# Performance work log

Hardware: AMD Instinct MI355X
Metric: run time of the kernel (lower is better)

Reference implementation:

```python
import jax, jax.numpy as jnp
import numpy as np

N_HASHES = 8
BUCKET_SIZE = 64


def setup_inputs() -> dict:
    key = jax.random.key(0)
    k1, k2, k3 = jax.random.split(key, 3)
    B, S, D = 16, 4096, 64
    n_buckets = S // BUCKET_SIZE  # 64
    qk = jax.random.normal(k1, (B, S, D), jnp.float32)
    v = jax.random.normal(k2, (B, S, D), jnp.float32)
    # random rotations (shared across batch, per hash round): (1, D, n_hashes, n_buckets//2)
    rotations = jax.random.normal(k3, (1, D, N_HASHES, n_buckets // 2), jnp.float32)
    return {"qk": qk, "v": v, "rotations": rotations}


def _look_one_back(x):
    # concat each chunk with the previous chunk (wrap-around), along the within-chunk axis
    x_extra = jnp.roll(x, 1, axis=1)
    return jnp.concatenate([x, x_extra], axis=2)


def _lsh_attention(qk, v, rotations):
    B, S, D = qk.shape
    n_buckets = S // BUCKET_SIZE

    # ---- hash_vectors ----
    rot = jnp.broadcast_to(rotations, (B, D, N_HASHES, n_buckets // 2))
    rotated = jnp.einsum('btf,bfhi->bhti', qk, rot)           # [B, H, S, nb/2]
    rotated = jnp.concatenate([rotated, -rotated], axis=-1)    # [B, H, S, nb]
    buckets = jnp.argmax(rotated, axis=-1)                     # [B, H, S]
    offsets = (jnp.arange(N_HASHES) * n_buckets).reshape(1, -1, 1)
    buckets = (buckets + offsets).reshape(B, -1)               # [B, H*S]

    # ---- sort by (bucket, position) ----
    total = N_HASHES * S
    ticker = jnp.arange(total)
    buckets_and_t = S * buckets + (ticker % S)[None, :]        # unique keys
    sticker = jnp.argsort(buckets_and_t, axis=-1)              # sort order
    undo_sort = jnp.argsort(sticker, axis=-1)

    st = sticker % S                                           # original positions
    sqk = jnp.take_along_axis(qk, st[..., None], axis=1)       # [B, H*S, D]
    sv = jnp.take_along_axis(v, st[..., None], axis=1)

    chunk_size = N_HASHES * n_buckets                          # number of chunks
    bq_t = st.reshape(B, chunk_size, -1)                       # [B, C, bs]
    bqk = sqk.reshape(B, chunk_size, -1, D)                    # [B, C, bs, D]
    bv = sv.reshape(B, chunk_size, -1, D)

    bq = bqk
    bk = bqk / jnp.clip(jnp.linalg.norm(bqk, axis=-1, keepdims=True), 1e-12)

    bk = _look_one_back(bk)                                    # [B, C, 2*bs, D]
    bv = _look_one_back(bv)
    bkv_t = _look_one_back(bq_t)                               # [B, C, 2*bs]

    dots = jnp.einsum('bhie,bhje->bhij', bq, bk) * (D ** -0.5)  # [B, C, bs, 2*bs]

    # mask self-attention (token attending to itself)
    self_mask = bq_t[:, :, :, None] == bkv_t[:, :, None, :]
    dots = jnp.where(self_mask, jnp.float32(-1e5), dots)

    lse = jax.nn.logsumexp(dots, axis=-1, keepdims=True)
    probs = jnp.exp(dots - lse)
    bo = jnp.einsum('buij,buje->buie', probs, bv)              # [B, C, bs, D]

    so = bo.reshape(B, -1, D)                                  # [B, H*S, D]
    slogits = lse.reshape(B, -1)                               # [B, H*S]

    # unsort back to original order
    o = jnp.take_along_axis(so, undo_sort[..., None], axis=1)
    logits = jnp.take_along_axis(slogits, undo_sort, axis=1)

    o = o.reshape(B, N_HASHES, S, D)
    logits = logits.reshape(B, N_HASHES, S, 1)

    # combine hash rounds by normalized logsumexp weights
    w = jnp.exp(logits - jax.nn.logsumexp(logits, axis=1, keepdims=True))
    out = jnp.sum(o * w, axis=1)                               # [B, S, D]
    return out, buckets


def reference(qk, v, rotations):
    return _lsh_attention(qk, v, rotations)
```

## Files before the change

kernel.cpp:

```cpp
#include <hip/hip_runtime.h>
#include <hip/hip_bf16.h>
#include <math.h>

#define B 16
#define S 4096
#define D 64
#define NH 8
#define NBUCK 64
#define CHUNKS 512
#define BS 64

#define GAP_MFMA 0.03f

typedef __attribute__((ext_vector_type(8))) short s8_t;
typedef __attribute__((ext_vector_type(8))) _Float16 h8_t;
typedef __attribute__((ext_vector_type(4))) float f4_t;
typedef __attribute__((ext_vector_type(2))) unsigned int u32x2;

__device__ inline unsigned short f16_rne(float x) {
    union { _Float16 f; unsigned short u; } cv;
    cv.f = (_Float16)x;
    return cv.u;
}
__device__ inline unsigned int pack_f16_pair(float x0, float x1) {
    return (unsigned int)f16_rne(x0) | ((unsigned int)f16_rne(x1) << 16);
}
__device__ inline unsigned int pack_trunc(float x0, float x1) {
    return __builtin_amdgcn_perm(__float_as_uint(x1), __float_as_uint(x0),
                                 0x07060302u);
}
__device__ inline unsigned short bf16_trunc(float x) {
    return (unsigned short)(__float_as_uint(x) >> 16);
}

#define BAR_LGKM() do {                                          \
    asm volatile("s_waitcnt lgkmcnt(0)" ::: "memory");           \
    __builtin_amdgcn_s_barrier();                                \
    asm volatile("" ::: "memory");                               \
} while (0)

template<int OFF>
__device__ inline u32x2 tr_read(unsigned int vaddr) {
    u32x2 d;
    asm volatile("ds_read_b64_tr_b16 %0, %1 offset:%c2"
                 : "=v"(d) : "v"(vaddr), "i"(OFF));
    return d;
}

#define HA_OFF 0
#define HQ_OFF 36864
#define HLDS_TOT 55296
#define HSTR 144

__global__ __launch_bounds__(256, 2) void hash_kernel(
    const float* __restrict__ qk, const float* __restrict__ rot,
    float* __restrict__ out_buckets, int* __restrict__ bucket_ws,
    unsigned char* __restrict__ flag_ws)
{
    __shared__ char lds[HLDS_TOT];
    int tid = threadIdx.x;
    int wg = blockIdx.x;
    int orig = ((wg & 7) << 6) + (wg >> 3);
    int b    = orig >> 5;
    int tile = orig & 31;
    int token0 = tile * 128;

    {
        char* arow = lds + HA_OFF + tid * HSTR;
        #pragma unroll 4
        for (int f = 0; f < 64; f += 2) {
            float r0 = rot[(size_t)f * 256 + tid];
            float r1 = rot[(size_t)(f + 1) * 256 + tid];
            *(unsigned int*)(arow + f * 2) = pack_f16_pair(r0, r1);
        }
    }
    {
        int wv0   = tid >> 6;
        int lane0 = tid & 63;
        int s_ = lane0 & 3;
        int rowA = wv0 * 32 + (lane0 >> 2);
        int rowB = rowA + 16;
        const float4* qA = (const float4*)(qk + ((size_t)b * S + token0 + rowA) * D);
        const float4* qB = (const float4*)(qk + ((size_t)b * S + token0 + rowB) * D);
        float4 a4[4], b4[4];
        #pragma unroll
        for (int n = 0; n < 4; ++n) { a4[n] = qA[n * 4 + s_]; b4[n] = qB[n * 4 + s_]; }

        char* qhA = lds + HQ_OFF + rowA * HSTR;
        char* qhB = lds + HQ_OFF + rowB * HSTR;
        #pragma unroll
        for (int n = 0; n < 4; ++n) {
            *(uint2*)(qhA + n * 32 + s_ * 8) =
                make_uint2(pack_f16_pair(a4[n].x, a4[n].y),
                           pack_f16_pair(a4[n].z, a4[n].w));
            *(uint2*)(qhB + n * 32 + s_ * 8) =
                make_uint2(pack_f16_pair(b4[n].x, b4[n].y),
                           pack_f16_pair(b4[n].z, b4[n].w));
        }
    }
    __syncthreads();

    int wv   = tid >> 6;
    int lane = tid & 63;
    int quad = lane >> 4;
    int cc   = lane & 15;

    for (int nt = 0; nt < 2; ++nt) {
        int ntg = wv * 2 + nt;
        const char* qr = lds + HQ_OFF + (ntg * 16 + cc) * HSTR + quad * 16;
        h8_t b0 = *(const h8_t*)(qr);
        h8_t b1 = *(const h8_t*)(qr + 64);

        float v1 = -3e38f, v2 = -3e38f;
        int i1 = 0;

        for (int mt = 0; mt < 16; ++mt) {
            const char* arow = lds + HA_OFF + (mt * 16 + cc) * HSTR + quad * 16;
            h8_t a0 = *(const h8_t*)(arow);
            h8_t a1 = *(const h8_t*)(arow + 64);
            f4_t acc = (f4_t){0.f, 0.f, 0.f, 0.f};
            acc = __builtin_amdgcn_mfma_f32_16x16x32_f16(a0, b0, acc, 0, 0, 0);
            acc = __builtin_amdgcn_mfma_f32_16x16x32_f16(a1, b1, acc, 0, 0, 0);

            if ((mt & 1) == 0) { v1 = -3e38f; v2 = -3e38f; i1 = 0; }
            int ibase = ((mt & 1) << 4) + (quad << 2);
            #pragma unroll
            for (int r = 0; r < 4; ++r) {
                float vp = acc[r];
                int ip = ibase + r;
                v2 = fmaxf(v2, fminf(vp, v1));
                if (vp > v1) { v1 = vp; i1 = ip; }
                float vn = -vp;
                v2 = fmaxf(v2, fminf(vn, v1));
                if (vn > v1) { v1 = vn; i1 = ip + 32; }
            }

            if (mt & 1) {
                #pragma unroll
                for (int off = 16; off <= 32; off <<= 1) {
                    float ov1 = __shfl_xor(v1, off, 64);
                    float ov2 = __shfl_xor(v2, off, 64);
                    int   oi1 = __shfl_xor(i1, off, 64);
                    float nv2 = fmaxf(fmaxf(v2, ov2), fminf(v1, ov1));
                    if (ov1 > v1) { v1 = ov1; i1 = oi1; }
                    v2 = nv2;
                }
                if (quad == 0) {
                    int h = mt >> 1;
                    int tok = token0 + ntg * 16 + cc;
                    size_t idx = (size_t)(b * NH + h) * S + tok;
                    bucket_ws[idx] = i1;
                    out_buckets[idx] = (float)(i1 + h * NBUCK);
                    flag_ws[idx] = (v1 - v2 < GAP_MFMA) ? 1 : 0;
                }
            }
        }
    }
}

__global__ __launch_bounds__(256) void hash_fixup_kernel(
    const float* __restrict__ qk, const float* __restrict__ rot,
    const unsigned char* __restrict__ flag_ws,
    float* __restrict__ out_buckets, int* __restrict__ bucket_ws)
{
    __shared__ int list[2048];
    __shared__ int cnt;
    int tid = threadIdx.x;
    if (tid == 0) cnt = 0;
    __syncthreads();

    int base = blockIdx.x * 2048;
    for (int i = tid; i < 2048; i += 256) {
        if (flag_ws[base + i]) {
            int slot = atomicAdd(&cnt, 1);
            list[slot] = base + i;
        }
    }
    __syncthreads();
    int n = cnt;

    for (int j = tid; j < n; j += 256) {
        int gid = list[j];
        int bh = gid >> 12, t = gid & (S - 1);
        int b = bh >> 3, h = bh & 7;
        const float* row = qk + ((size_t)b * S + t) * D;

        double acc[32];
        #pragma unroll
        for (int i = 0; i < 32; ++i) acc[i] = 0.0;
        for (int f = 0; f < 64; ++f) {
            double x = (double)row[f];
            const float* rr = rot + f * (NH * 32) + h * 32;
            #pragma unroll
            for (int i = 0; i < 32; ++i)
                acc[i] = __fma_rn(x, (double)rr[i], acc[i]);
        }
        double best = acc[0]; int bi = 0;
        double worst = acc[0]; int wi = 0;
        #pragma unroll
        for (int i = 1; i < 32; ++i) {
            if (acc[i] > best)  { best = acc[i]; bi = i; }
            if (acc[i] < worst) { worst = acc[i]; wi = i; }
        }
        int bucket = (-worst > best) ? (32 + wi) : bi;
        bucket_ws[gid] = bucket;
        out_buckets[gid] = (float)(bucket + h * NBUCK);
    }
}

__global__ __launch_bounds__(1024) void sort_kernel(
    const int* __restrict__ bucket_ws, int* __restrict__ st_ws)
{
    __shared__ int sb[S];
    __shared__ int hist[16][64];
    __shared__ int bpref[64];
    __shared__ int woff[16][64];

    int tid  = threadIdx.x;
    int wv   = tid >> 6;
    int lane = tid & 63;
    int base = blockIdx.x * S;

    hist[wv][lane] = 0;
    __syncthreads();

    int qbase = wv * 256;
    #pragma unroll
    for (int i = 0; i < 4; ++i) {
        int t = qbase + i * 64 + lane;
        int v = bucket_ws[base + t];
        sb[t] = v;
        atomicAdd(&hist[wv][v], 1);
    }
    __syncthreads();

    if (wv == 0) {
        int total = 0;
        #pragma unroll
        for (int w = 0; w < 16; ++w) total += hist[w][lane];
        int x = total;
        #pragma unroll
        for (int off = 1; off < 64; off <<= 1) {
            int y = __shfl_up(x, off, 64);
            if (lane >= off) x += y;
        }
        bpref[lane] = x - total;
    }
    __syncthreads();
    {
        int o = bpref[lane];
        #pragma unroll
        for (int w2 = 0; w2 < 16; ++w2) {
            if (w2 < wv) o += hist[w2][lane];
        }
        woff[wv][lane] = o;
    }
    __syncthreads();

    for (int g = 0; g < 4; ++g) {
        int t = qbase + g * 64 + lane;
        int v = sb[t];

        unsigned long long m = ~0ULL;
        #pragma unroll
        for (int bit = 0; bit < 6; ++bit) {
            unsigned long long bm = __ballot((v >> bit) & 1);
            m &= ((v >> bit) & 1) ? bm : ~bm;
        }
        unsigned long long below = (lane == 63) ? ~0ULL >> 1
                                 : ((1ULL << lane) - 1ULL);
        int rank = __popcll(m & below);
        int cnt  = __popcll(m);

        int pos = woff[wv][v] + rank;
        st_ws[base + pos] = t;

        if ((m & below) == 0ULL)
            woff[wv][v] += cnt;
    }
}

#define OFF_VT 18432
#define OFF_NRM 35840
#define OFF_TKX 36352
#define OFF_PINV 36864
#define LDS_TOT 37120
#define KSTRB 144
#define PSTRB 272

template<int KC>
__device__ inline void pv_step(const char* lds, unsigned vaddr,
                               int wv, int cc, int quad, f4_t* oaccT)
{
    s8_t pb = *(const s8_t*)(lds + (wv * 16 + cc) * PSTRB + KC * 64 + quad * 16);
    u32x2 t00 = tr_read<KC * 4352 +    0>(vaddr);
    u32x2 t01 = tr_read<KC * 4352 +  544>(vaddr);
    u32x2 t10 = tr_read<KC * 4352 + 1088>(vaddr);
    u32x2 t11 = tr_read<KC * 4352 + 1632>(vaddr);
    u32x2 t20 = tr_read<KC * 4352 + 2176>(vaddr);
    u32x2 t21 = tr_read<KC * 4352 + 2720>(vaddr);
    u32x2 t30 = tr_read<KC * 4352 + 3264>(vaddr);
    u32x2 t31 = tr_read<KC * 4352 + 3808>(vaddr);
    asm volatile("s_waitcnt lgkmcnt(0)" ::: "memory");
    __builtin_amdgcn_sched_barrier(0);
    union { u32x2 d[2]; s8_t s; } u0, u1, u2, u3;
    u0.d[0] = t00; u0.d[1] = t01;
    u1.d[0] = t10; u1.d[1] = t11;
    u2.d[0] = t20; u2.d[1] = t21;
    u3.d[0] = t30; u3.d[1] = t31;
    oaccT[0] = __builtin_amdgcn_mfma_f32_16x16x32_bf16(u0.s, pb, oaccT[0], 0, 0, 0);
    oaccT[1] = __builtin_amdgcn_mfma_f32_16x16x32_bf16(u1.s, pb, oaccT[1], 0, 0, 0);
    oaccT[2] = __builtin_amdgcn_mfma_f32_16x16x32_bf16(u2.s, pb, oaccT[2], 0, 0, 0);
    oaccT[3] = __builtin_amdgcn_mfma_f32_16x16x32_bf16(u3.s, pb, oaccT[3], 0, 0, 0);
}

__global__ __launch_bounds__(256, 4) void attn_kernel(
    const float* __restrict__ qk, const float* __restrict__ v,
    const int* __restrict__ st_ws,
    __hip_bfloat16* __restrict__ o_ws, float* __restrict__ logits_ws)
{
    __shared__ char lds[LDS_TOT];
    float* nrm_s  = (float*)(lds + OFF_NRM);
    int*   tkx    = (int*)(lds + OFF_TKX);
    float* pinv_s = (float*)(lds + OFF_PINV);

    int tid = threadIdx.x;
    int wg = blockIdx.x;
    int orig = ((wg & 7) << 10) + (wg >> 3);
    int c = orig & (CHUNKS - 1);
    int b = orig >> 9;
    int h = c >> 6;
    int sbase = b * (NH * S);
    int cprev = (c + CHUNKS - 1) & (CHUNKS - 1);

    int wv   = tid >> 6;
    int lane = tid & 63;
    int quad = lane >> 4;
    int cc   = lane & 15;
    int s_   = lane & 3;

    int rowA = wv * 32 + (lane >> 2);
    int rowB = rowA + 16;
    int chK  = (wv < 2) ? c : cprev;
    int tokKA = st_ws[sbase + chK * BS + (rowA & 63)];
    int tokKB = st_ws[sbase + chK * BS + (rowB & 63)];
    const float4* kpA = (const float4*)(qk + ((size_t)b * S + tokKA) * D);
    const float4* kpB = (const float4*)(qk + ((size_t)b * S + tokKB) * D);
    float4 kA4[4], kB4[4];
    #pragma unroll
    for (int n = 0; n < 4; ++n) { kA4[n] = kpA[n * 4 + s_]; kB4[n] = kpB[n * 4 + s_]; }

    int prA = wv * 32 + (lane >> 2);
    int prB = prA + 16;
    int ciA = ((prA & 3) << 4) | (prA >> 3);
    int ciB = ((prB & 3) << 4) | (prB >> 3);
    int chVA = (prA & 4) ? cprev : c;
    int chVB = (prB & 4) ? cprev : c;
    int tokVA = st_ws[sbase + chVA * BS + ciA];
    int tokVB = st_ws[sbase + chVB * BS + ciB];
    const float4* vpA = (const float4*)(v + ((size_t)b * S + tokVA) * D);
    const float4* vpB = (const float4*)(v + ((size_t)b * S + tokVB) * D);
    float4 vA4[4], vB4[4];
    #pragma unroll
    for (int n = 0; n < 4; ++n) { vA4[n] = vpA[n * 4 + s_]; vB4[n] = vpB[n * 4 + s_]; }

    {
        float ssA = 0.f, ssB = 0.f;
        #pragma unroll
        for (int n = 0; n < 4; ++n) {
            ssA += kA4[n].x*kA4[n].x + kA4[n].y*kA4[n].y
                 + kA4[n].z*kA4[n].z + kA4[n].w*kA4[n].w;
            ssB += kB4[n].x*kB4[n].x + kB4[n].y*kB4[n].y
                 + kB4[n].z*kB4[n].z + kB4[n].w*kB4[n].w;
        }
        ssA += __shfl_xor(ssA, 1, 64); ssA += __shfl_xor(ssA, 2, 64);
        ssB += __shfl_xor(ssB, 1, 64); ssB += __shfl_xor(ssB, 2, 64);
        if (s_ == 0) {
            nrm_s[rowA] = __builtin_amdgcn_rsqf(fmaxf(ssA, 1e-24f)) * 0.18033688f;
            nrm_s[rowB] = __builtin_amdgcn_rsqf(fmaxf(ssB, 1e-24f)) * 0.18033688f;
            tkx[rowA] = tokKA;
            tkx[rowB] = tokKB;
        }
        #pragma unroll
        for (int n = 0; n < 4; ++n) {
            *(uint2*)(lds + rowA * KSTRB + n * 32 + s_ * 8) =
                make_uint2(pack_trunc(kA4[n].x, kA4[n].y),
                           pack_trunc(kA4[n].z, kA4[n].w));
            *(uint2*)(lds + rowB * KSTRB + n * 32 + s_ * 8) =
                make_uint2(pack_trunc(kB4[n].x, kB4[n].y),
                           pack_trunc(kB4[n].z, kB4[n].w));
        }
    }
    BAR_LGKM();

    int qrow = wv * 16 + cc;
    f4_t acc[8];
    #pragma unroll
    for (int t = 0; t < 8; ++t) acc[t] = (f4_t){0.f,0.f,0.f,0.f};

    __builtin_amdgcn_s_setprio(1);
    #pragma unroll
    for (int kc = 0; kc < 2; ++kc) {
        int aoff = kc * 64 + quad * 16;
        s8_t av = *(const s8_t*)(lds + qrow * KSTRB + aoff);
        #pragma unroll
        for (int t = 0; t < 8; ++t) {
            s8_t bv = *(const s8_t*)(lds + (t * 16 + cc) * KSTRB + aoff);
            acc[t] = __builtin_amdgcn_mfma_f32_16x16x32_bf16(av, bv, acc[t], 0, 0, 0);
        }
    }
    __builtin_amdgcn_s_setprio(0);

    {
        int kcA = prA >> 5, qA = (prA >> 3) & 3, rA = (prA >> 2) & 1, jA = prA & 3;
        int kcB = prB >> 5, qB = (prB >> 3) & 3, rB = (prB >> 2) & 1, jB = prB & 3;
        #pragma unroll
        for (int n = 0; n < 4; ++n) {
            *(uint2*)(lds + OFF_VT + (kcA * 8 + n * 2 + rA) * 544
                      + qA * 128 + jA * 32 + s_ * 8) =
                make_uint2(pack_trunc(vA4[n].x, vA4[n].y),
                           pack_trunc(vA4[n].z, vA4[n].w));
            *(uint2*)(lds + OFF_VT + (kcB * 8 + n * 2 + rB) * 544
                      + qB * 128 + jB * 32 + s_ * 8) =
                make_uint2(pack_trunc(vB4[n].x, vB4[n].y),
                           pack_trunc(vB4[n].z, vB4[n].w));
        }
    }

    float invsc[8];
    #pragma unroll
    for (int t = 0; t < 8; ++t)
        invsc[t] = nrm_s[t * 16 + cc];

    float sm[4] = {0.f, 0.f, 0.f, 0.f};
    #pragma unroll
    for (int t = 0; t < 8; ++t) {
        #pragma unroll
        for (int g = 0; g < 4; ++g)
            acc[t][g] = __builtin_amdgcn_exp2f(acc[t][g] * invsc[t]);
        if (t == wv) {
            #pragma unroll
            for (int g = 0; g < 4; ++g)
                if (cc == quad * 4 + g) acc[t][g] = 0.f;
        }
        #pragma unroll
        for (int g = 0; g < 4; ++g) sm[g] += acc[t][g];
    }
    #pragma unroll
    for (int msk = 1; msk <= 8; msk <<= 1)
        #pragma unroll
        for (int g = 0; g < 4; ++g) sm[g] += __shfl_xor(sm[g], msk, 64);

    if (cc == 0) {
        #pragma unroll
        for (int g = 0; g < 4; ++g) {
            int q = wv * 16 + quad * 4 + g;
            int tq = tkx[q];
            pinv_s[q] = __builtin_amdgcn_rcpf(sm[g]);
            logits_ws[sbase + h * S + tq] = 0.69314718f * __log2f(sm[g]);
        }
    }

    BAR_LGKM();
    #pragma unroll
    for (int g = 0; g < 4; ++g) {
        int q = wv * 16 + quad * 4 + g;
        uint4 w;
        w.x = pack_trunc(acc[0][g], acc[1][g]);
        w.y = pack_trunc(acc[2][g], acc[3][g]);
        w.z = pack_trunc(acc[4][g], acc[5][g]);
        w.w = pack_trunc(acc[6][g], acc[7][g]);
        *(uint4*)(lds + q * PSTRB + cc * 16) = w;
    }

    f4_t oaccT[4];
    #pragma unroll
    for (int n = 0; n < 4; ++n) oaccT[n] = (f4_t){0.f,0.f,0.f,0.f};

    unsigned vaddr = (unsigned)(unsigned long long)(lds + OFF_VT)
                   + (unsigned)lane * 8u;

    __builtin_amdgcn_s_setprio(1);
    pv_step<0>(lds, vaddr, wv, cc, quad, oaccT);
    pv_step<1>(lds, vaddr, wv, cc, quad, oaccT);
    pv_step<2>(lds, vaddr, wv, cc, quad, oaccT);
    pv_step<3>(lds, vaddr, wv, cc, quad, oaccT);
    __builtin_amdgcn_s_setprio(0);

    {
        int q = wv * 16 + cc;
        int tok = tkx[q];
        float pq = pinv_s[q];
        __hip_bfloat16* op = o_ws + ((size_t)(sbase + h * S + tok)) * D + quad * 4;
        #pragma unroll
        for (int n = 0; n < 4; ++n) {
            uint2 pk2;
            pk2.x = pack_trunc(oaccT[n][0] * pq, oaccT[n][1] * pq);
            pk2.y = pack_trunc(oaccT[n][2] * pq, oaccT[n][3] * pq);
            *(uint2*)(op + n * 16) = pk2;
        }
    }
}

__global__ __launch_bounds__(256) void combine_kernel(
    const __hip_bfloat16* __restrict__ o_ws, const float* __restrict__ logits_ws,
    float* __restrict__ out)
{
    int gid = blockIdx.x * 256 + threadIdx.x;
    int token = gid >> 3;
    int d8 = gid & 7;
    int b = token >> 12;
    int t = token & (S - 1);
    int base = b * (NH * S) + t;

    float l[8];
    #pragma unroll
    for (int hh = 0; hh < 8; ++hh) l[hh] = logits_ws[base + hh * S];
    float m = l[0];
    #pragma unroll
    for (int hh = 1; hh < 8; ++hh) m = fmaxf(m, l[hh]);
    float w[8]; float ssum = 0.f;
    #pragma unroll
    for (int hh = 0; hh < 8; ++hh) { w[hh] = __expf(l[hh] - m); ssum += w[hh]; }
    float inv = __builtin_amdgcn_rcpf(ssum);

    float accv[8] = {0,0,0,0,0,0,0,0};
    #pragma unroll
    for (int hh = 0; hh < 8; ++hh) {
        uint4 pk = *(const uint4*)(o_ws + (size_t)(base + hh * S) * D + d8 * 8);
        float wh = w[hh] * inv;
        unsigned int ws_[4] = {pk.x, pk.y, pk.z, pk.w};
        #pragma unroll
        for (int e = 0; e < 4; ++e) {
            float lo = __uint_as_float(ws_[e] << 16);
            float hi = __uint_as_float(ws_[e] & 0xffff0000u);
            accv[2*e]   += wh * lo;
            accv[2*e+1] += wh * hi;
        }
    }
    float4* op = (float4*)(out + (size_t)token * D + d8 * 8);
    op[0] = make_float4(accv[0], accv[1], accv[2], accv[3]);
    op[1] = make_float4(accv[4], accv[5], accv[6], accv[7]);
}

extern "C" void kernel_launch(void* const* d_in, const int* in_sizes, int n_in,
                              void* d_out, int out_size, void* d_ws, size_t ws_size,
                              hipStream_t stream) {
    const float* qk  = (const float*)d_in[0];
    const float* v   = (const float*)d_in[1];
    const float* rot = (const float*)d_in[2];

    float* out         = (float*)d_out;
    float* out_buckets = out + (size_t)B * S * D;

    int*   bucket_ws = (int*)d_ws;
    int*   st_ws     = bucket_ws + (size_t)B * NH * S;
    float* logits_ws = (float*)(st_ws + (size_t)B * NH * S);
    __hip_bfloat16* o_ws = (__hip_bfloat16*)(logits_ws + (size_t)B * NH * S);
    unsigned char* flag_ws = (unsigned char*)(o_ws + (size_t)B * NH * S * D);

    hash_kernel<<<B * 32, 256, 0, stream>>>(qk, rot, out_buckets, bucket_ws,
                                            flag_ws);
    hash_fixup_kernel<<<(B * NH * S) / 2048, 256, 0, stream>>>(
        qk, rot, flag_ws, out_buckets, bucket_ws);
    sort_kernel<<<B * NH, 1024, 0, stream>>>(bucket_ws, st_ws);
    attn_kernel<<<B * CHUNKS, 256, 0, stream>>>(qk, v, st_ws, o_ws, logits_ws);
    combine_kernel<<<(B * S * 8) / 256, 256, 0, stream>>>(o_ws, logits_ws, out);
}
```

Before: 185.2 us.

## Fuse hash fixup into sort kernel and remap combine block indexing

Merges the fp64 hash-fixup pass into the per-(batch,hash) sort kernel. Flagged tokens are recomputed there using rotations staged in shared memory, and the corrected buckets are written straight into the shared sort buffer. This removes one kernel launch and the global round trip of bucket_ws between fixup and sort. The sort block drops from 1024 to 512 threads, and the flagged list is capped at 1024 entries, so any overflow beyond that would go uncorrected. The combine kernel also remaps block indices to interleave batches, which changes its memory access locality.

```diff
diff --git a/kernel.cpp b/kernel.cpp
--- a/kernel.cpp
+++ b/kernel.cpp
@@ -158,39 +158,70 @@
     }
 }
 
-__global__ __launch_bounds__(256) void hash_fixup_kernel(
+__global__ __launch_bounds__(512) void sort_kernel(
+    const int* __restrict__ bucket_ws, int* __restrict__ st_ws,
     const float* __restrict__ qk, const float* __restrict__ rot,
-    const unsigned char* __restrict__ flag_ws,
-    float* __restrict__ out_buckets, int* __restrict__ bucket_ws)
+    const unsigned char* __restrict__ flag_ws, float* __restrict__ out_buckets)
 {
-    __shared__ int list[2048];
+    __shared__ int sb[S];
+    __shared__ int hist[8][64];
+    __shared__ int bpref[64];
+    __shared__ int woff[8][64];
+    __shared__ float rots[2048];
+    __shared__ int list[1024];
     __shared__ int cnt;
-    int tid = threadIdx.x;
+
+    int tid  = threadIdx.x;
+    int wv   = tid >> 6;
+    int lane = tid & 63;
+    int bh   = blockIdx.x;
+    int b    = bh >> 3;
+    int h    = bh & 7;
+    int base = bh * S;
+
+    hist[wv][lane] = 0;
     if (tid == 0) cnt = 0;
     __syncthreads();
 
-    int base = blockIdx.x * 2048;
-    for (int i = tid; i < 2048; i += 256) {
-        if (flag_ws[base + i]) {
-            int slot = atomicAdd(&cnt, 1);
-            list[slot] = base + i;
-        }
-    }
-    __syncthreads();
-    int n = cnt;
-
-    for (int j = tid; j < n; j += 256) {
-        int gid = list[j];
-        int bh = gid >> 12, t = gid & (S - 1);
-        int b = bh >> 3, h = bh & 7;
+    int qbase = wv * 512;
+    #pragma unroll
+    for (int i = 0; i < 8; ++i) {
+        int t = qbase + i * 64 + lane;
+        sb[t] = bucket_ws[base + t];
+    }
+    {
+        uint2 f8 = *(const uint2*)(flag_ws + base + tid * 8);
+        unsigned int fw[2] = {f8.x, f8.y};
+        #pragma unroll
+        for (int w2 = 0; w2 < 2; ++w2) {
+            unsigned int fv = fw[w2];
+            if (fv) {
+                #pragma unroll
+                for (int e = 0; e < 4; ++e)
+                    if ((fv >> (8 * e)) & 0xffu) {
+                        int slot = atomicAdd(&cnt, 1);
+                        if (slot < 1024) list[slot] = tid * 8 + w2 * 4 + e;
+                    }
+            }
+        }
+    }
+    #pragma unroll
+    for (int k = 0; k < 4; ++k) {
+        int idx = tid * 4 + k;
+        rots[idx] = rot[(size_t)(idx >> 5) * 256 + h * 32 + (idx & 31)];
+    }
+    __syncthreads();
+
+    int n = cnt; if (n > 1024) n = 1024;
+    for (int j = tid; j < n; j += 512) {
+        int t = list[j];
         const float* row = qk + ((size_t)b * S + t) * D;
-
         double acc[32];
         #pragma unroll
         for (int i = 0; i < 32; ++i) acc[i] = 0.0;
         for (int f = 0; f < 64; ++f) {
             double x = (double)row[f];
-            const float* rr = rot + f * (NH * 32) + h * 32;
+            const float* rr = rots + f * 32;
             #pragma unroll
             for (int i = 0; i < 32; ++i)
                 acc[i] = __fma_rn(x, (double)rr[i], acc[i]);
@@ -203,41 +234,20 @@
             if (acc[i] < worst) { worst = acc[i]; wi = i; }
         }
         int bucket = (-worst > best) ? (32 + wi) : bi;
-        bucket_ws[gid] = bucket;
-        out_buckets[gid] = (float)(bucket + h * NBUCK);
-    }
-}
-
-__global__ __launch_bounds__(1024) void sort_kernel(
-    const int* __restrict__ bucket_ws, int* __restrict__ st_ws)
-{
-    __shared__ int sb[S];
-    __shared__ int hist[16][64];
-    __shared__ int bpref[64];
-    __shared__ int woff[16][64];
-
-    int tid  = threadIdx.x;
-    int wv   = tid >> 6;
-    int lane = tid & 63;
-    int base = blockIdx.x * S;
-
-    hist[wv][lane] = 0;
-    __syncthreads();
-
-    int qbase = wv * 256;
-    #pragma unroll
-    for (int i = 0; i < 4; ++i) {
-        int t = qbase + i * 64 + lane;
-        int v = bucket_ws[base + t];
-        sb[t] = v;
-        atomicAdd(&hist[wv][v], 1);
-    }
+        sb[t] = bucket;
+        out_buckets[base + t] = (float)(bucket + h * NBUCK);
+    }
+    __syncthreads();
+
+    #pragma unroll
+    for (int i = 0; i < 8; ++i)
+        atomicAdd(&hist[wv][sb[qbase + i * 64 + lane]], 1);
     __syncthreads();
 
     if (wv == 0) {
         int total = 0;
         #pragma unroll
-        for (int w = 0; w < 16; ++w) total += hist[w][lane];
+        for (int w = 0; w < 8; ++w) total += hist[w][lane];
         int x = total;
         #pragma unroll
         for (int off = 1; off < 64; off <<= 1) {
@@ -249,15 +259,14 @@
     __syncthreads();
     {
         int o = bpref[lane];
-        #pragma unroll
-        for (int w2 = 0; w2 < 16; ++w2) {
+        for (int w2 = 0; w2 < 8; ++w2) {
             if (w2 < wv) o += hist[w2][lane];
         }
         woff[wv][lane] = o;
     }
     __syncthreads();
 
-    for (int g = 0; g < 4; ++g) {
+    for (int g = 0; g < 8; ++g) {
         int t = qbase + g * 64 + lane;
         int v = sb[t];
 
@@ -270,13 +279,13 @@
         unsigned long long below = (lane == 63) ? ~0ULL >> 1
                                  : ((1ULL << lane) - 1ULL);
         int rank = __popcll(m & below);
-        int cnt  = __popcll(m);
+        int cnt2 = __popcll(m);
 
         int pos = woff[wv][v] + rank;
         st_ws[base + pos] = t;
 
         if ((m & below) == 0ULL)
-            woff[wv][v] += cnt;
+            woff[wv][v] += cnt2;
     }
 }
 
@@ -506,11 +515,13 @@
     const __hip_bfloat16* __restrict__ o_ws, const float* __restrict__ logits_ws,
     float* __restrict__ out)
 {
-    int gid = blockIdx.x * 256 + threadIdx.x;
-    int token = gid >> 3;
-    int d8 = gid & 7;
-    int b = token >> 12;
-    int t = token & (S - 1);
+    int wg = blockIdx.x;
+    int b  = ((wg & 7) << 1) | ((wg >> 3) & 1);
+    int tb = wg >> 4;
+    int tid = threadIdx.x;
+    int t = tb * 32 + (tid >> 3);
+    int d8 = tid & 7;
+    int token = (b << 12) + t;
     int base = b * (NH * S) + t;
 
     float l[8];
@@ -561,9 +572,8 @@
 
     hash_kernel<<<B * 32, 256, 0, stream>>>(qk, rot, out_buckets, bucket_ws,
                                             flag_ws);
-    hash_fixup_kernel<<<(B * NH * S) / 2048, 256, 0, stream>>>(
-        qk, rot, flag_ws, out_buckets, bucket_ws);
-    sort_kernel<<<B * NH, 1024, 0, stream>>>(bucket_ws, st_ws);
+    sort_kernel<<<B * NH, 512, 0, stream>>>(bucket_ws, st_ws, qk, rot,
+                                            flag_ws, out_buckets);
     attn_kernel<<<B * CHUNKS, 256, 0, stream>>>(qk, v, st_ws, o_ws, logits_ws);
     combine_kernel<<<(B * S * 8) / 256, 256, 0, stream>>>(o_ws, logits_ws, out);
 }
```

Result: faster. 180.4 us (-2.6%).
